# Optimization experiments

Measured on AMD Instinct MI355X. Metric: run time of the kernel, lower is better.

Reference implementation:

```python
import jax, jax.numpy as jnp
import numpy as np

N_TOKEN = 32000; N_LAYER = 6; N_HEAD = 16; D_MODEL = 1024; D_HEAD = 64; D_INNER = 4096
QLEN = 512; MEM_LEN = 512; BSZ = 4


def setup_inputs() -> dict:
    key = jax.random.key(0)
    ks = jax.random.split(key, 12)
    f = lambda k, shape: jax.random.normal(k, shape, dtype=jnp.float32) * 0.02
    return {
        'data': jax.random.randint(ks[0], (QLEN, BSZ), 0, N_TOKEN, dtype=jnp.int32),
        'target': jax.random.randint(ks[1], (QLEN, BSZ), 0, N_TOKEN, dtype=jnp.int32),
        'mems': jax.random.normal(ks[2], (N_LAYER + 1, MEM_LEN, BSZ, D_MODEL), dtype=jnp.float32),
        'emb_weight': f(ks[3], (N_TOKEN, D_MODEL)),        # tied input/output embedding
        'out_bias': jnp.zeros((N_TOKEN,), jnp.float32),
        'r_w_bias': f(ks[4], (N_HEAD, D_HEAD)),
        'r_r_bias': f(ks[5], (N_HEAD, D_HEAD)),
        'qkv_w': f(ks[6], (N_LAYER, 3 * N_HEAD * D_HEAD, D_MODEL)),  # bias=False in original
        'r_w': f(ks[7], (N_LAYER, N_HEAD * D_HEAD, D_MODEL)),        # r_net, bias=False
        'o_w': f(ks[8], (N_LAYER, D_MODEL, N_HEAD * D_HEAD)),        # o_net, bias=False
        'ln1_g': jnp.ones((N_LAYER, D_MODEL), jnp.float32),
        'ln1_b': jnp.zeros((N_LAYER, D_MODEL), jnp.float32),
        'ff1_w': f(ks[9], (N_LAYER, D_INNER, D_MODEL)),
        'ff1_b': jnp.zeros((N_LAYER, D_INNER), jnp.float32),
        'ff2_w': f(ks[10], (N_LAYER, D_MODEL, D_INNER)),
        'ff2_b': jnp.zeros((N_LAYER, D_MODEL), jnp.float32),
        'ln2_g': jnp.ones((N_LAYER, D_MODEL), jnp.float32),
        'ln2_b': jnp.zeros((N_LAYER, D_MODEL), jnp.float32),
    }


def _layernorm(x, g, b, eps=1e-5):
    mu = x.mean(-1, keepdims=True)
    var = ((x - mu) ** 2).mean(-1, keepdims=True)
    return (x - mu) * jax.lax.rsqrt(var + eps) * g + b


def _rel_shift(x):
    # x: (qlen, klen, bsz, n_head) -> TransformerXL relative shift
    q, k, b, h = x.shape
    x = jnp.concatenate([jnp.zeros((q, 1, b, h), x.dtype), x], axis=1)  # (q, k+1, b, h)
    return x.reshape(k + 1, q, b, h)[1:].reshape(q, k, b, h)


def _forward_core(data, target, mems, emb_weight, out_bias, r_w_bias, r_r_bias,
                  qkv_w, r_w, o_w, ln1_g, ln1_b, ff1_w, ff1_b, ff2_w, ff2_b, ln2_g, ln2_b):
    qlen, bsz = data.shape
    mlen = mems.shape[1]
    klen = mlen + qlen
    scale = 1.0 / (D_HEAD ** 0.5)

    # AdaptiveEmbedding with div_val=1, no cutoffs: plain lookup scaled by sqrt(d_model)
    h = emb_weight[data] * jnp.float32(D_MODEL ** 0.5)  # (qlen, bsz, d_model)

    # sinusoidal relative positions, descending klen-1 .. 0
    pos_seq = jnp.arange(klen - 1, -1, -1, dtype=jnp.float32)
    inv_freq = 1.0 / (10000.0 ** (jnp.arange(0, D_MODEL, 2, dtype=jnp.float32) / D_MODEL))
    sinusoid = pos_seq[:, None] * inv_freq[None, :]
    pos_emb = jnp.concatenate([jnp.sin(sinusoid), jnp.cos(sinusoid)], axis=-1)  # (klen, d_model)

    # causal mask shifted by memory length
    attn_mask = jnp.triu(jnp.ones((qlen, klen), bool), k=1 + mlen)
    NEG = jnp.float32(-1e30)

    for i in range(N_LAYER):
        cat = jnp.concatenate([mems[i], h], axis=0)              # (klen, b, d)
        heads = jnp.einsum('kbd,ed->kbe', cat, qkv_w[i])         # (klen, b, 3*H*dh)
        q, k_, v = jnp.split(heads, 3, axis=-1)
        q = q[-qlen:].reshape(qlen, bsz, N_HEAD, D_HEAD)
        k_ = k_.reshape(klen, bsz, N_HEAD, D_HEAD)
        v = v.reshape(klen, bsz, N_HEAD, D_HEAD)
        r = jnp.einsum('kd,ed->ke', pos_emb, r_w[i]).reshape(klen, N_HEAD, D_HEAD)

        AC = jnp.einsum('ibnd,jbnd->ijbn', q + r_w_bias, k_)     # content term
        BD = _rel_shift(jnp.einsum('ibnd,jnd->ijbn', q + r_r_bias, r))  # position term
        score = (AC + BD) * scale
        score = jnp.where(attn_mask[:, :, None, None], NEG, score)
        prob = jax.nn.softmax(score, axis=1)                     # over key axis j
        attn_vec = jnp.einsum('ijbn,jbnd->ibnd', prob, v).reshape(qlen, bsz, N_HEAD * D_HEAD)
        attn_out = jnp.einsum('ibe,de->ibd', attn_vec, o_w[i])
        h = _layernorm(h + attn_out, ln1_g[i], ln1_b[i])         # post-lnorm (pre_lnorm=False)

        ff_h = jax.nn.relu(jnp.einsum('ibd,fd->ibf', h, ff1_w[i]) + ff1_b[i])
        ff = jnp.einsum('ibf,df->ibd', ff_h, ff2_w[i]) + ff2_b[i]
        h = _layernorm(h + ff, ln2_g[i], ln2_b[i])

    # ProjectedAdaptiveLogSoftmax, no cutoffs, tied weight: plain softmax NLL
    logits = jnp.einsum('ibd,vd->ibv', h, emb_weight) + out_bias
    logp = jax.nn.log_softmax(logits, axis=-1)
    loss = -jnp.take_along_axis(logp, target[:, :, None].astype(jnp.int32), axis=-1)[:, :, 0]
    return loss  # (tgt_len, bsz)


def reference(data, target, mems, emb_weight, out_bias, r_w_bias, r_r_bias,
              qkv_w, r_w, o_w, ln1_g, ln1_b, ff1_w, ff1_b, ff2_w, ff2_b, ln2_g, ln2_b):
    return _forward_core(data, target, mems, emb_weight, out_bias, r_w_bias, r_r_bias,
                         qkv_w, r_w, o_w, ln1_g, ln1_b, ff1_w, ff1_b, ff2_w, ff2_b, ln2_g, ln2_b)
```

## Files before the change

kernel.cpp:

```cpp
#include <hip/hip_runtime.h>
#include <math.h>


typedef unsigned short u16;
typedef __attribute__((ext_vector_type(8))) short bf16x8;
typedef __attribute__((ext_vector_type(4))) float f32x4;

#define LINMOD (1 << 30)
constexpr int PITCH = 40;

__device__ __forceinline__ u16 f2bf(float f) {
    unsigned u = __float_as_uint(f);
    return (u16)((u + 0x7fffu + ((u >> 16) & 1u)) >> 16);
}
__device__ __forceinline__ float bf2f(u16 b) {
    return __uint_as_float((unsigned)b << 16);
}

template<int BM, int BN, int EPI>
__global__ __launch_bounds__(256)
void mgemm(const u16* __restrict__ A, int lda, long alo, long ahi, int amod,
           const u16* __restrict__ B, int ldb, long blo, long bhi, int bmod,
           void* __restrict__ Cv, int ldc, long clo, long chi, int cmod,
           const float* __restrict__ bias, int M, int N, int K, int relu)
{
    constexpr int WM = BM / 2, WN = BN / 2, MT = WM / 16, NT = WN / 16;
    __shared__ u16 As[BM * PITCH];
    __shared__ u16 Bs[BN * PITCH];
    const int z = blockIdx.z;
    A += (long)(z % amod) * alo + (long)(z / amod) * ahi;
    B += (long)(z % bmod) * blo + (long)(z / bmod) * bhi;
    const long coff = (long)(z % cmod) * clo + (long)(z / cmod) * chi;

    const int m0 = blockIdx.y * BM, n0 = blockIdx.x * BN;
    const int t = threadIdx.x;
    const int l = t & 63, w = t >> 6;
    const int wm = w >> 1, wn = w & 1;
    const int fr = l & 15, fq = l >> 4;

    f32x4 acc[MT][NT];
    #pragma unroll
    for (int i = 0; i < MT; ++i)
        #pragma unroll
        for (int j = 0; j < NT; ++j) acc[i][j] = (f32x4){0.f, 0.f, 0.f, 0.f};

    constexpr int AIT = BM * 4 / 256;
    constexpr int BIT = BN * 4 / 256;

    const int nk = K / 32;
    for (int kt = 0; kt < nk; ++kt) {
        uint4 av[AIT], bv[BIT];
        #pragma unroll
        for (int i = 0; i < AIT; ++i) {
            int c = t + i * 256, row = c >> 2, q = c & 3;
            av[i] = *(const uint4*)(A + (long)(m0 + row) * lda + kt * 32 + q * 8);
        }
        #pragma unroll
        for (int i = 0; i < BIT; ++i) {
            int c = t + i * 256, row = c >> 2, q = c & 3;
            bv[i] = *(const uint4*)(B + (long)(n0 + row) * ldb + kt * 32 + q * 8);
        }
        __syncthreads();
        #pragma unroll
        for (int i = 0; i < AIT; ++i) {
            int c = t + i * 256, row = c >> 2, q = c & 3;
            *(uint4*)&As[row * PITCH + q * 8] = av[i];
        }
        #pragma unroll
        for (int i = 0; i < BIT; ++i) {
            int c = t + i * 256, row = c >> 2, q = c & 3;
            *(uint4*)&Bs[row * PITCH + q * 8] = bv[i];
        }
        __syncthreads();
        bf16x8 af[MT], bfr[NT];
        #pragma unroll
        for (int i = 0; i < MT; ++i)
            af[i] = *(const bf16x8*)&As[(wm * WM + i * 16 + fr) * PITCH + fq * 8];
        #pragma unroll
        for (int j = 0; j < NT; ++j)
            bfr[j] = *(const bf16x8*)&Bs[(wn * WN + j * 16 + fr) * PITCH + fq * 8];
        #pragma unroll
        for (int i = 0; i < MT; ++i)
            #pragma unroll
            for (int j = 0; j < NT; ++j)
                acc[i][j] = __builtin_amdgcn_mfma_f32_16x16x32_bf16(
                    af[i], bfr[j], acc[i][j], 0, 0, 0);
    }

    if constexpr (EPI == 1) {
        u16* C = (u16*)Cv + coff;
        #pragma unroll
        for (int i = 0; i < MT; ++i) {
            int rb = m0 + wm * WM + i * 16 + fq * 4;
            #pragma unroll
            for (int j = 0; j < NT; ++j) {
                int gcol = n0 + wn * WN + j * 16 + fr;
                float bb = bias ? bias[gcol] : 0.f;
                #pragma unroll
                for (int r = 0; r < 4; ++r) {
                    float v = acc[i][j][r] + bb;
                    if (relu) v = fmaxf(v, 0.f);
                    C[(long)(rb + r) * ldc + gcol] = f2bf(v);
                }
            }
        }
    } else {
        float* C = (float*)Cv + coff;
        #pragma unroll
        for (int i = 0; i < MT; ++i) {
            int rb = m0 + wm * WM + i * 16 + fq * 4;
            #pragma unroll
            for (int j = 0; j < NT; ++j) {
                int gcol = n0 + wn * WN + j * 16 + fr;
                float bb = bias ? bias[gcol] : 0.f;
                #pragma unroll
                for (int r = 0; r < 4; ++r) {
                    float v = acc[i][j][r] + bb;
                    if (relu) v = fmaxf(v, 0.f);
                    C[(long)(rb + r) * ldc + gcol] = v;
                }
            }
        }
    }
}

template<int BM, int BN, int EPI>
static inline void mg(hipStream_t st,
    const u16* A, int lda, long alo, long ahi, int amod,
    const u16* B, int ldb, long blo, long bhi, int bmod,
    void* C, int ldc, long clo, long chi, int cmod,
    const float* bias, int M, int N, int K, int relu, int batch)
{
    dim3 grid(N / BN, M / BM, batch);
    mgemm<BM, BN, EPI><<<grid, 256, 0, st>>>(A, lda, alo, ahi, amod,
        B, ldb, blo, bhi, bmod, C, ldc, clo, chi, cmod, bias, M, N, K, relu);
}

__global__ __launch_bounds__(256)
void attn_kernel(const u16* __restrict__ qw, const u16* __restrict__ qr,
                 const u16* __restrict__ heads, const u16* __restrict__ rbuf,
                 u16* __restrict__ attnv)
{
    __shared__ u16 sm[80384];
    __shared__ float pmax[2][128];
    __shared__ float psum[2][128];
    u16* qw_s = sm;
    u16* qr_s = sm + 9216;
    u16* k_s  = sm + 18432;
    u16* r_s  = sm + 27648;
    u16* vT_s = sm + 36864;
    u16* bd0  = sm + 45568;
    u16* bd1  = sm + 62976;

    const int zz = blockIdx.x, b = zz >> 4, n = zz & 15;
    const int i0 = blockIdx.y * 128;
    const int t = threadIdx.x, l = t & 63, w = t >> 6;
    const int fr = l & 15, fq = l >> 4, wm = w >> 1, wn = w & 1;

    const u16* qwg = qw + (long)zz * 32768 + (long)i0 * 64;
    const u16* qrg = qr + (long)zz * 32768 + (long)i0 * 64;
    {
        int jr0 = 384 - i0;
        #pragma unroll
        for (int it = 0; it < 4; ++it) {
            int idx = t + it * 256, row = idx >> 3, q8 = idx & 7;
            *(uint4*)&qw_s[row * 72 + q8 * 8] = *(const uint4*)&qwg[row * 64 + q8 * 8];
            *(uint4*)&qr_s[row * 72 + q8 * 8] = *(const uint4*)&qrg[row * 64 + q8 * 8];
            *(uint4*)&r_s[row * 72 + q8 * 8] =
                *(const uint4*)&rbuf[(long)(jr0 + row) * 1024 + n * 64 + q8 * 8];
        }
    }
    __syncthreads();

    auto computeBD = [&](u16* out) {
        f32x4 bacc[4][4];
        #pragma unroll
        for (int i = 0; i < 4; ++i)
            #pragma unroll
            for (int j = 0; j < 4; ++j) bacc[i][j] = (f32x4){0.f, 0.f, 0.f, 0.f};
        #pragma unroll
        for (int ks = 0; ks < 2; ++ks) {
            bf16x8 af[4], bfr[4];
            #pragma unroll
            for (int i = 0; i < 4; ++i)
                af[i] = *(const bf16x8*)&qr_s[(wm * 64 + i * 16 + fr) * 72 + ks * 32 + fq * 8];
            #pragma unroll
            for (int j = 0; j < 4; ++j)
                bfr[j] = *(const bf16x8*)&r_s[(wn * 64 + j * 16 + fr) * 72 + ks * 32 + fq * 8];
            #pragma unroll
            for (int i = 0; i < 4; ++i)
                #pragma unroll
                for (int j = 0; j < 4; ++j)
                    bacc[i][j] = __builtin_amdgcn_mfma_f32_16x16x32_bf16(
                        af[i], bfr[j], bacc[i][j], 0, 0, 0);
        }
        #pragma unroll
        for (int i = 0; i < 4; ++i)
            #pragma unroll
            for (int j = 0; j < 4; ++j)
                #pragma unroll
                for (int r = 0; r < 4; ++r)
                    out[(wm * 64 + i * 16 + fq * 4 + r) * 136 + wn * 64 + j * 16 + fr] =
                        f2bf(bacc[i][j][r]);
    };
    computeBD(bd0);

    float m_st[4][4], l_st[4][4];
    #pragma unroll
    for (int i = 0; i < 4; ++i)
        #pragma unroll
        for (int r = 0; r < 4; ++r) { m_st[i][r] = -3e38f; l_st[i][r] = 0.f; }
    f32x4 Oa[4][2];
    #pragma unroll
    for (int i = 0; i < 4; ++i)
        #pragma unroll
        for (int j = 0; j < 2; ++j) Oa[i][j] = (f32x4){0.f, 0.f, 0.f, 0.f};

    const int ntiles = (640 + i0) >> 7;
    for (int tt = 0; tt < ntiles; ++tt) {
        const int j0 = tt << 7;
        const int jr0b = j0 - i0 + 512;
        u16* bda = (tt & 1) ? bd1 : bd0;
        u16* bdb = (tt & 1) ? bd0 : bd1;

        __syncthreads();

        #pragma unroll
        for (int it = 0; it < 4; ++it) {
            int idx = t + it * 256, row = idx >> 3, q8 = idx & 7;
            long hb = ((long)(j0 + row) * 4 + b) * 3072 + n * 64 + q8 * 8;
            *(uint4*)&k_s[row * 72 + q8 * 8] = *(const uint4*)&heads[hb + 1024];
            uint4 vv = *(const uint4*)&heads[hb + 2048];
            u16 vt[8]; *(uint4*)vt = vv;
            #pragma unroll
            for (int d = 0; d < 8; ++d) vT_s[(q8 * 8 + d) * 136 + row] = vt[d];
            if (jr0b < 1024)
                *(uint4*)&r_s[row * 72 + q8 * 8] =
                    *(const uint4*)&rbuf[(long)(jr0b + row) * 1024 + n * 64 + q8 * 8];
        }
        __syncthreads();

        if (jr0b < 1024) computeBD(bdb);

        f32x4 acc[4][4];
        #pragma unroll
        for (int i = 0; i < 4; ++i)
            #pragma unroll
            for (int j = 0; j < 4; ++j) acc[i][j] = (f32x4){0.f, 0.f, 0.f, 0.f};
        #pragma unroll
        for (int ks = 0; ks < 2; ++ks) {
            bf16x8 af[4], bfr[4];
            #pragma unroll
            for (int i = 0; i < 4; ++i)
                af[i] = *(const bf16x8*)&qw_s[(wm * 64 + i * 16 + fr) * 72 + ks * 32 + fq * 8];
            #pragma unroll
            for (int j = 0; j < 4; ++j)
                bfr[j] = *(const bf16x8*)&k_s[(wn * 64 + j * 16 + fr) * 72 + ks * 32 + fq * 8];
            #pragma unroll
            for (int i = 0; i < 4; ++i)
                #pragma unroll
                for (int j = 0; j < 4; ++j)
                    acc[i][j] = __builtin_amdgcn_mfma_f32_16x16x32_bf16(
                        af[i], bfr[j], acc[i][j], 0, 0, 0);
        }
        __syncthreads();

        const int Dl = j0 - i0;
        float rm[4][4];
        #pragma unroll
        for (int i = 0; i < 4; ++i)
            #pragma unroll
            for (int r = 0; r < 4; ++r) rm[i][r] = -3e38f;
        #pragma unroll
        for (int i = 0; i < 4; ++i) {
            #pragma unroll
            for (int r = 0; r < 4; ++r) {
                int ii = wm * 64 + i * 16 + fq * 4 + r;
                #pragma unroll
                for (int j = 0; j < 4; ++j) {
                    int jj = wn * 64 + j * 16 + fr;
                    int d = jj - ii;
                    int idx = 127 + d;
                    u16 bv = (idx < 128) ? bda[ii * 136 + idx] : bdb[ii * 136 + idx - 128];
                    float sv = (acc[i][j][r] + bf2f(bv)) * 0.125f;
                    sv = (Dl + d > 512) ? -1e30f : sv;
                    acc[i][j][r] = sv;
                    rm[i][r] = fmaxf(rm[i][r], sv);
                }
            }
        }
        #pragma unroll
        for (int i = 0; i < 4; ++i)
            #pragma unroll
            for (int r = 0; r < 4; ++r) {
                float v = rm[i][r];
                v = fmaxf(v, __shfl_xor(v, 1, 64));
                v = fmaxf(v, __shfl_xor(v, 2, 64));
                v = fmaxf(v, __shfl_xor(v, 4, 64));
                v = fmaxf(v, __shfl_xor(v, 8, 64));
                rm[i][r] = v;
            }
        if (fr == 0) {
            #pragma unroll
            for (int i = 0; i < 4; ++i)
                #pragma unroll
                for (int r = 0; r < 4; ++r)
                    pmax[wn][wm * 64 + i * 16 + fq * 4 + r] = rm[i][r];
        }
        __syncthreads();

        float alpha[4][4];
        #pragma unroll
        for (int i = 0; i < 4; ++i)
            #pragma unroll
            for (int r = 0; r < 4; ++r) {
                int row = wm * 64 + i * 16 + fq * 4 + r;
                float tm = fmaxf(pmax[0][row], pmax[1][row]);
                float mn = fmaxf(m_st[i][r], tm);
                alpha[i][r] = __expf(m_st[i][r] - mn);
                m_st[i][r] = mn;
            }
        u16* Pp = bda;
        float rs[4][4];
        #pragma unroll
        for (int i = 0; i < 4; ++i)
            #pragma unroll
            for (int r = 0; r < 4; ++r) rs[i][r] = 0.f;
        #pragma unroll
        for (int i = 0; i < 4; ++i) {
            #pragma unroll
            for (int r = 0; r < 4; ++r) {
                int row = wm * 64 + i * 16 + fq * 4 + r;
                #pragma unroll
                for (int j = 0; j < 4; ++j) {
                    float p = __expf(acc[i][j][r] - m_st[i][r]);
                    rs[i][r] += p;
                    Pp[row * 136 + wn * 64 + j * 16 + fr] = f2bf(p);
                }
            }
        }
        #pragma unroll
        for (int i = 0; i < 4; ++i)
            #pragma unroll
            for (int r = 0; r < 4; ++r) {
                float v = rs[i][r];
                v += __shfl_xor(v, 1, 64);
                v += __shfl_xor(v, 2, 64);
                v += __shfl_xor(v, 4, 64);
                v += __shfl_xor(v, 8, 64);
                rs[i][r] = v;
            }
        if (fr == 0) {
            #pragma unroll
            for (int i = 0; i < 4; ++i)
                #pragma unroll
                for (int r = 0; r < 4; ++r)
                    psum[wn][wm * 64 + i * 16 + fq * 4 + r] = rs[i][r];
        }
        #pragma unroll
        for (int i = 0; i < 4; ++i)
            #pragma unroll
            for (int j = 0; j < 2; ++j)
                #pragma unroll
                for (int r = 0; r < 4; ++r) Oa[i][j][r] *= alpha[i][r];
        __syncthreads();

        #pragma unroll
        for (int i = 0; i < 4; ++i)
            #pragma unroll
            for (int r = 0; r < 4; ++r) {
                int row = wm * 64 + i * 16 + fq * 4 + r;
                l_st[i][r] = alpha[i][r] * l_st[i][r] + psum[0][row] + psum[1][row];
            }
        #pragma unroll
        for (int ks = 0; ks < 4; ++ks) {
            bf16x8 pa[4], vb[2];
            #pragma unroll
            for (int i = 0; i < 4; ++i)
                pa[i] = *(const bf16x8*)&Pp[(wm * 64 + i * 16 + fr) * 136 + ks * 32 + fq * 8];
            #pragma unroll
            for (int j = 0; j < 2; ++j)
                vb[j] = *(const bf16x8*)&vT_s[(wn * 32 + j * 16 + fr) * 136 + ks * 32 + fq * 8];
            #pragma unroll
            for (int i = 0; i < 4; ++i)
                #pragma unroll
                for (int j = 0; j < 2; ++j)
                    Oa[i][j] = __builtin_amdgcn_mfma_f32_16x16x32_bf16(
                        pa[i], vb[j], Oa[i][j], 0, 0, 0);
        }
    }

    #pragma unroll
    for (int i = 0; i < 4; ++i) {
        #pragma unroll
        for (int r = 0; r < 4; ++r) {
            int gi = i0 + wm * 64 + i * 16 + fq * 4 + r;
            float inv = 1.0f / l_st[i][r];
            #pragma unroll
            for (int j = 0; j < 2; ++j) {
                int col = n * 64 + wn * 32 + j * 16 + fr;
                attnv[((long)gi * 4 + b) * 1024 + col] = f2bf(Oa[i][j][r] * inv);
            }
        }
    }
}


__device__ __forceinline__ float blk_sum(float v, float* smv) {
    #pragma unroll
    for (int m = 32; m; m >>= 1) v += __shfl_xor(v, m, 64);
    int lane = threadIdx.x & 63, w = threadIdx.x >> 6;
    if (lane == 0) smv[w] = v;
    __syncthreads();
    v = smv[0] + smv[1] + smv[2] + smv[3];
    __syncthreads();
    return v;
}

__device__ __forceinline__ float blk_max(float v, float* smv) {
    #pragma unroll
    for (int m = 32; m; m >>= 1) v = fmaxf(v, __shfl_xor(v, m, 64));
    int lane = threadIdx.x & 63, w = threadIdx.x >> 6;
    if (lane == 0) smv[w] = v;
    __syncthreads();
    v = fmaxf(fmaxf(smv[0], smv[1]), fmaxf(smv[2], smv[3]));
    __syncthreads();
    return v;
}

__global__ __launch_bounds__(256)
void f2b_kernel(const float* __restrict__ in, u16* __restrict__ out, int n4)
{
    int i = blockIdx.x * 256 + threadIdx.x;
    if (i >= n4) return;
    float4 v = ((const float4*)in)[i];
    uint2 o;
    o.x = (unsigned)f2bf(v.x) | ((unsigned)f2bf(v.y) << 16);
    o.y = (unsigned)f2bf(v.z) | ((unsigned)f2bf(v.w) << 16);
    ((uint2*)out)[i] = o;
}

__global__ __launch_bounds__(256)
void cat_kernel(const float* __restrict__ memsl, const float* __restrict__ h,
                u16* __restrict__ cat)
{
    int i = blockIdx.x * 256 + threadIdx.x;
    float4 v = (i < 524288) ? ((const float4*)memsl)[i]
                            : ((const float4*)h)[i - 524288];
    uint2 o;
    o.x = (unsigned)f2bf(v.x) | ((unsigned)f2bf(v.y) << 16);
    o.y = (unsigned)f2bf(v.z) | ((unsigned)f2bf(v.w) << 16);
    ((uint2*)cat)[i] = o;
}

__global__ __launch_bounds__(256)
void embed_kernel(const int* __restrict__ data, const float* __restrict__ emb,
                  float* __restrict__ h)
{
    long idx = (long)blockIdx.x * 256 + threadIdx.x;
    int r = (int)(idx >> 10), d = (int)(idx & 1023);
    h[idx] = emb[(long)data[r] * 1024 + d] * 32.0f;
}

__global__ __launch_bounds__(256)
void posemb_kernel(u16* __restrict__ pe)
{
    int idx = blockIdx.x * 256 + threadIdx.x;
    int p = idx >> 10, d = idx & 1023;
    float pos = (float)(1023 - p);
    int j = d & 511;
    float invf = powf(10000.0f, -(float)j * (1.0f / 512.0f));
    float a = pos * invf;
    pe[idx] = f2bf((d < 512) ? sinf(a) : cosf(a));
}

__global__ __launch_bounds__(256)
void qwqr_kernel(const u16* __restrict__ heads, const float* __restrict__ rwb,
                 const float* __restrict__ rrb, u16* __restrict__ qw,
                 u16* __restrict__ qr)
{
    int idx = blockIdx.x * 256 + threadIdx.x;
    int d = idx & 63, i = (idx >> 6) & 511, n = (idx >> 15) & 15, b = idx >> 19;
    float v = bf2f(heads[(long)((512 + i) * 4 + b) * 3072 + n * 64 + d]);
    int e = n * 64 + d;
    qw[idx] = f2bf(v + rwb[e]);
    qr[idx] = f2bf(v + rrb[e]);
}

__global__ __launch_bounds__(256)
void add_ln_kernel(float* __restrict__ h, const float* __restrict__ res,
                   const float* __restrict__ g, const float* __restrict__ be)
{
    __shared__ float smv[4];
    int row = blockIdx.x, t = threadIdx.x;
    float* hp = h + (long)row * 1024;
    float4 x = *(float4*)(hp + t * 4);
    float4 rv = *(const float4*)(res + (long)row * 1024 + t * 4);
    x.x += rv.x; x.y += rv.y; x.z += rv.z; x.w += rv.w;
    float s = blk_sum(x.x + x.y + x.z + x.w, smv);
    float mu = s * (1.0f / 1024.0f);
    float d0 = x.x - mu, d1 = x.y - mu, d2 = x.z - mu, d3 = x.w - mu;
    float s2 = blk_sum(d0 * d0 + d1 * d1 + d2 * d2 + d3 * d3, smv);
    float inv = rsqrtf(s2 * (1.0f / 1024.0f) + 1e-5f);
    float4 gg = *(const float4*)(g + t * 4);
    float4 bb = *(const float4*)(be + t * 4);
    float4 o;
    o.x = d0 * inv * gg.x + bb.x;
    o.y = d1 * inv * gg.y + bb.y;
    o.z = d2 * inv * gg.z + bb.z;
    o.w = d3 * inv * gg.w + bb.w;
    *(float4*)(hp + t * 4) = o;
}

__global__ void init_ms_kernel(float2* __restrict__ ms)
{
    int i = blockIdx.x * 256 + threadIdx.x;
    if (i < 2048) ms[i] = make_float2(-3e38f, 0.f);
}

__global__ __launch_bounds__(256)
void merge_kernel(const float* __restrict__ chunk, float2* __restrict__ ms, int CN)
{
    __shared__ float smv[4];
    int row = blockIdx.x, t = threadIdx.x;
    const float* cp = chunk + (long)row * CN;
    float m = -3e38f;
    for (int j = t; j < CN; j += 256) m = fmaxf(m, cp[j]);
    m = blk_max(m, smv);
    float s = 0.f;
    for (int j = t; j < CN; j += 256) s += __expf(cp[j] - m);
    s = blk_sum(s, smv);
    if (t == 0) {
        float2 cur = ms[row];
        float nm = fmaxf(cur.x, m);
        ms[row] = make_float2(nm, cur.y * __expf(cur.x - nm) + s * __expf(m - nm));
    }
}

__global__ __launch_bounds__(256)
void final_kernel(const float* __restrict__ h, const float* __restrict__ emb,
                  const float* __restrict__ ob, const int* __restrict__ target,
                  const float2* __restrict__ ms, float* __restrict__ out)
{
    __shared__ float smv[4];
    int row = blockIdx.x, t = threadIdx.x;
    int tok = target[row];
    const float* hp = h + (long)row * 1024;
    const float* ep = emb + (long)tok * 1024;
    float4 a = *(const float4*)(hp + t * 4);
    float4 b = *(const float4*)(ep + t * 4);
    float s = blk_sum(a.x * b.x + a.y * b.y + a.z * b.z + a.w * b.w, smv);
    if (t == 0) {
        float2 v = ms[row];
        out[row] = v.x + logf(v.y) - (s + ob[tok]);
    }
}


extern "C" void kernel_launch(void* const* d_in, const int* in_sizes, int n_in,
                              void* d_out, int out_size, void* d_ws, size_t ws_size,
                              hipStream_t stream)
{
    const int*   data     = (const int*)d_in[0];
    const int*   target   = (const int*)d_in[1];
    const float* mems     = (const float*)d_in[2];
    const float* emb      = (const float*)d_in[3];
    const float* out_bias = (const float*)d_in[4];
    const float* r_w_bias = (const float*)d_in[5];
    const float* r_r_bias = (const float*)d_in[6];
    const float* qkv_w    = (const float*)d_in[7];
    const float* r_w      = (const float*)d_in[8];
    const float* o_w      = (const float*)d_in[9];
    const float* ln1_g    = (const float*)d_in[10];
    const float* ln1_b    = (const float*)d_in[11];
    const float* ff1_w    = (const float*)d_in[12];
    const float* ff1_b    = (const float*)d_in[13];
    const float* ff2_w    = (const float*)d_in[14];
    const float* ff2_b    = (const float*)d_in[15];
    const float* ln2_g    = (const float*)d_in[16];
    const float* ln2_b    = (const float*)d_in[17];
    float* out = (float*)d_out;
    float* ws  = (float*)d_ws;

    float* h       = ws;
    float* tmp     = ws + 2097152;
    u16*  pe_bf    = (u16*)(ws + 4194304);
    u16*  rbuf_bf  = (u16*)(ws + 4718592);
    u16*  cat_bf   = (u16*)(ws + 5242880);
    u16*  heads_bf = (u16*)(ws + 7340032);
    u16*  qw_bf    = (u16*)(ws + 13631488);
    u16*  qr_bf    = (u16*)(ws + 14680064);
    u16*  attnv_bf = (u16*)(ws + 15728640);
    u16*  h_bf     = (u16*)(ws + 16777216);
    u16*  wqkv     = (u16*)(ws + 17825792);
    u16*  wr       = wqkv + 3145728;
    u16*  wo       = wr + 1048576;
    u16*  wf1      = wo + 1048576;
    u16*  wf2      = wf1 + 4194304;
    float* big     = ws + 24641536;
    float2* ms     = (float2*)(ws + 58195968);
    u16*  ffh_bf   = (u16*)big;
    float* chunk   = big;
    u16*  embc_bf  = (u16*)(big + 16777216);

    embed_kernel<<<8192, 256, 0, stream>>>(data, emb, h);
    posemb_kernel<<<4096, 256, 0, stream>>>(pe_bf);

    for (int l = 0; l < 6; ++l) {
        f2b_kernel<<<3072, 256, 0, stream>>>(qkv_w + (size_t)l * 3145728, wqkv, 786432);
        f2b_kernel<<<1024, 256, 0, stream>>>(r_w + (size_t)l * 1048576, wr, 262144);
        f2b_kernel<<<1024, 256, 0, stream>>>(o_w + (size_t)l * 1048576, wo, 262144);
        f2b_kernel<<<4096, 256, 0, stream>>>(ff1_w + (size_t)l * 4194304, wf1, 1048576);
        f2b_kernel<<<4096, 256, 0, stream>>>(ff2_w + (size_t)l * 4194304, wf2, 1048576);
        cat_kernel<<<4096, 256, 0, stream>>>(mems + (size_t)l * 2097152, h, cat_bf);

        mg<128,128,1>(stream, cat_bf, 1024, 0, 0, LINMOD, wqkv, 1024, 0, 0, LINMOD,
                      heads_bf, 3072, 0, 0, LINMOD, nullptr, 4096, 3072, 1024, 0, 1);
        mg<64,64,1>(stream, pe_bf, 1024, 0, 0, LINMOD, wr, 1024, 0, 0, LINMOD,
                    rbuf_bf, 1024, 0, 0, LINMOD, nullptr, 1024, 1024, 1024, 0, 1);

        qwqr_kernel<<<8192, 256, 0, stream>>>(heads_bf, r_w_bias, r_r_bias, qw_bf, qr_bf);

        attn_kernel<<<dim3(64, 4), 256, 0, stream>>>(qw_bf, qr_bf, heads_bf,
                                                     rbuf_bf, attnv_bf);

        mg<64,64,0>(stream, attnv_bf, 1024, 0, 0, LINMOD, wo, 1024, 0, 0, LINMOD,
                    tmp, 1024, 0, 0, LINMOD, nullptr, 2048, 1024, 1024, 0, 1);

        add_ln_kernel<<<2048, 256, 0, stream>>>(h, tmp, ln1_g + l * 1024, ln1_b + l * 1024);
        f2b_kernel<<<2048, 256, 0, stream>>>(h, h_bf, 524288);

        mg<64,64,1>(stream, h_bf, 1024, 0, 0, LINMOD, wf1, 1024, 0, 0, LINMOD,
                    ffh_bf, 4096, 0, 0, LINMOD, ff1_b + l * 4096, 2048, 4096, 1024, 1, 1);
        mg<64,64,0>(stream, ffh_bf, 4096, 0, 0, LINMOD, wf2, 4096, 0, 0, LINMOD,
                    tmp, 1024, 0, 0, LINMOD, ff2_b + l * 1024, 2048, 1024, 4096, 0, 1);

        add_ln_kernel<<<2048, 256, 0, stream>>>(h, tmp, ln2_g + l * 1024, ln2_b + l * 1024);
    }

    f2b_kernel<<<2048, 256, 0, stream>>>(h, h_bf, 524288);
    init_ms_kernel<<<8, 256, 0, stream>>>(ms);

    const int chunkN[4] = {8192, 8192, 8192, 7424};
    long off = 0;
    for (int c = 0; c < 4; ++c) {
        int CN = chunkN[c];
        int n4 = CN * 1024 / 4;
        f2b_kernel<<<(n4 + 255) / 256, 256, 0, stream>>>(emb + off * 1024, embc_bf, n4);
        mg<128,128,0>(stream, h_bf, 1024, 0, 0, LINMOD, embc_bf, 1024, 0, 0, LINMOD,
                      chunk, CN, 0, 0, LINMOD, out_bias + off, 2048, CN, 1024, 0, 1);
        merge_kernel<<<2048, 256, 0, stream>>>(chunk, ms, CN);
        off += CN;
    }
    final_kernel<<<2048, 256, 0, stream>>>(h, emb, out_bias, target, ms, out);
}
```

Measured before the change: 3.482 ms.

## Fuse logits softmax partials into GEMM epilogue, retile GEMMs, add XCD swizzle

Adds a GEMM epilogue that reduces each 128-column logit tile to a per-row (max, sum-exp) pair. The full fp32 logits matrix is no longer written and reread in four chunks, and a small lse_kernel merges the 250 partials per row. It also enlarges tiles for the o/ff1/ff2 GEMMs and adds an XCD-aware workgroup remap for better L2 locality across MI355X chiplets. The whole embedding is now converted to bf16 in one pass, which needs a larger workspace region.

```diff
diff --git a/kernel.cpp b/kernel.cpp
--- a/kernel.cpp
+++ b/kernel.cpp
@@ -22,7 +22,7 @@
 void mgemm(const u16* __restrict__ A, int lda, long alo, long ahi, int amod,
            const u16* __restrict__ B, int ldb, long blo, long bhi, int bmod,
            void* __restrict__ Cv, int ldc, long clo, long chi, int cmod,
-           const float* __restrict__ bias, int M, int N, int K, int relu)
+           const float* __restrict__ bias, int M, int N, int K, int relu, int swz)
 {
     constexpr int WM = BM / 2, WN = BN / 2, MT = WM / 16, NT = WN / 16;
     __shared__ u16 As[BM * PITCH];
@@ -32,7 +32,16 @@
     B += (long)(z % bmod) * blo + (long)(z / bmod) * bhi;
     const long coff = (long)(z % cmod) * clo + (long)(z / cmod) * chi;
 
-    const int m0 = blockIdx.y * BM, n0 = blockIdx.x * BN;
+    int bx = blockIdx.x, by = blockIdx.y;
+    if (swz) {
+        int nwg = gridDim.x * gridDim.y;
+        int flat = by * gridDim.x + bx;
+        int q = nwg >> 3, rr = nwg & 7, xcd = flat & 7, idx = flat >> 3;
+        int wgid = (xcd < rr ? xcd * (q + 1) : rr * (q + 1) + (xcd - rr) * q) + idx;
+        by = wgid % gridDim.y;
+        bx = wgid / gridDim.y;
+    }
+    const int m0 = by * BM, n0 = bx * BN;
     const int t = threadIdx.x;
     const int l = t & 63, w = t >> 6;
     const int wm = w >> 1, wn = w & 1;
@@ -104,7 +113,7 @@
                 }
             }
         }
-    } else {
+    } else if constexpr (EPI == 0) {
         float* C = (float*)Cv + coff;
         #pragma unroll
         for (int i = 0; i < MT; ++i) {
@@ -121,6 +130,46 @@
                 }
             }
         }
+    } else {
+        __shared__ float pm[2][BM];
+        __shared__ float ps[2][BM];
+        float bb[NT];
+        #pragma unroll
+        for (int j = 0; j < NT; ++j)
+            bb[j] = bias ? bias[n0 + wn * WN + j * 16 + fr] : 0.f;
+        #pragma unroll
+        for (int i = 0; i < MT; ++i) {
+            #pragma unroll
+            for (int r = 0; r < 4; ++r) {
+                float mx = -3e38f;
+                #pragma unroll
+                for (int j = 0; j < NT; ++j) mx = fmaxf(mx, acc[i][j][r] + bb[j]);
+                mx = fmaxf(mx, __shfl_xor(mx, 1, 64));
+                mx = fmaxf(mx, __shfl_xor(mx, 2, 64));
+                mx = fmaxf(mx, __shfl_xor(mx, 4, 64));
+                mx = fmaxf(mx, __shfl_xor(mx, 8, 64));
+                float s = 0.f;
+                #pragma unroll
+                for (int j = 0; j < NT; ++j) s += __expf(acc[i][j][r] + bb[j] - mx);
+                s += __shfl_xor(s, 1, 64);
+                s += __shfl_xor(s, 2, 64);
+                s += __shfl_xor(s, 4, 64);
+                s += __shfl_xor(s, 8, 64);
+                if (fr == 0) {
+                    int row = wm * WM + i * 16 + fq * 4 + r;
+                    pm[wn][row] = mx;
+                    ps[wn][row] = s;
+                }
+            }
+        }
+        __syncthreads();
+        if (t < BM && (m0 + t) < M) {
+            float ma = pm[0][t], mb = pm[1][t];
+            float m = fmaxf(ma, mb);
+            float s = ps[0][t] * __expf(ma - m) + ps[1][t] * __expf(mb - m);
+            float2* P = (float2*)Cv;
+            P[(long)(m0 + t) * gridDim.x + bx] = make_float2(m, s);
+        }
     }
 }
 
@@ -129,11 +178,11 @@
     const u16* A, int lda, long alo, long ahi, int amod,
     const u16* B, int ldb, long blo, long bhi, int bmod,
     void* C, int ldc, long clo, long chi, int cmod,
-    const float* bias, int M, int N, int K, int relu, int batch)
+    const float* bias, int M, int N, int K, int relu, int batch, int swz)
 {
     dim3 grid(N / BN, M / BM, batch);
     mgemm<BM, BN, EPI><<<grid, 256, 0, st>>>(A, lda, alo, ahi, amod,
-        B, ldb, blo, bhi, bmod, C, ldc, clo, chi, cmod, bias, M, N, K, relu);
+        B, ldb, blo, bhi, bmod, C, ldc, clo, chi, cmod, bias, M, N, K, relu, swz);
 }
 
 __global__ __launch_bounds__(256)
@@ -512,29 +561,22 @@
     *(float4*)(hp + t * 4) = o;
 }
 
-__global__ void init_ms_kernel(float2* __restrict__ ms)
-{
-    int i = blockIdx.x * 256 + threadIdx.x;
-    if (i < 2048) ms[i] = make_float2(-3e38f, 0.f);
-}
-
-__global__ __launch_bounds__(256)
-void merge_kernel(const float* __restrict__ chunk, float2* __restrict__ ms, int CN)
+__global__ __launch_bounds__(256)
+void lse_kernel(const float2* __restrict__ part, int nblk, float2* __restrict__ ms)
 {
     __shared__ float smv[4];
     int row = blockIdx.x, t = threadIdx.x;
-    const float* cp = chunk + (long)row * CN;
+    const float2* pp = part + (long)row * nblk;
     float m = -3e38f;
-    for (int j = t; j < CN; j += 256) m = fmaxf(m, cp[j]);
+    for (int j = t; j < nblk; j += 256) m = fmaxf(m, pp[j].x);
     m = blk_max(m, smv);
     float s = 0.f;
-    for (int j = t; j < CN; j += 256) s += __expf(cp[j] - m);
+    for (int j = t; j < nblk; j += 256) {
+        float2 p = pp[j];
+        s += p.y * __expf(p.x - m);
+    }
     s = blk_sum(s, smv);
-    if (t == 0) {
-        float2 cur = ms[row];
-        float nm = fmaxf(cur.x, m);
-        ms[row] = make_float2(nm, cur.y * __expf(cur.x - nm) + s * __expf(m - nm));
-    }
+    if (t == 0) ms[row] = make_float2(m, s);
 }
 
 __global__ __launch_bounds__(256)
@@ -600,8 +642,8 @@
     float* big     = ws + 24641536;
     float2* ms     = (float2*)(ws + 58195968);
     u16*  ffh_bf   = (u16*)big;
-    float* chunk   = big;
-    u16*  embc_bf  = (u16*)(big + 16777216);
+    u16*  embc_bf  = (u16*)big;
+    float2* partials = (float2*)(big + 16777216);
 
     embed_kernel<<<8192, 256, 0, stream>>>(data, emb, h);
     posemb_kernel<<<4096, 256, 0, stream>>>(pe_bf);
@@ -615,42 +657,35 @@
         cat_kernel<<<4096, 256, 0, stream>>>(mems + (size_t)l * 2097152, h, cat_bf);
 
         mg<128,128,1>(stream, cat_bf, 1024, 0, 0, LINMOD, wqkv, 1024, 0, 0, LINMOD,
-                      heads_bf, 3072, 0, 0, LINMOD, nullptr, 4096, 3072, 1024, 0, 1);
+                      heads_bf, 3072, 0, 0, LINMOD, nullptr, 4096, 3072, 1024, 0, 1, 1);
         mg<64,64,1>(stream, pe_bf, 1024, 0, 0, LINMOD, wr, 1024, 0, 0, LINMOD,
-                    rbuf_bf, 1024, 0, 0, LINMOD, nullptr, 1024, 1024, 1024, 0, 1);
+                    rbuf_bf, 1024, 0, 0, LINMOD, nullptr, 1024, 1024, 1024, 0, 1, 0);
 
         qwqr_kernel<<<8192, 256, 0, stream>>>(heads_bf, r_w_bias, r_r_bias, qw_bf, qr_bf);
 
         attn_kernel<<<dim3(64, 4), 256, 0, stream>>>(qw_bf, qr_bf, heads_bf,
                                                      rbuf_bf, attnv_bf);
 
-        mg<64,64,0>(stream, attnv_bf, 1024, 0, 0, LINMOD, wo, 1024, 0, 0, LINMOD,
-                    tmp, 1024, 0, 0, LINMOD, nullptr, 2048, 1024, 1024, 0, 1);
+        mg<128,64,0>(stream, attnv_bf, 1024, 0, 0, LINMOD, wo, 1024, 0, 0, LINMOD,
+                     tmp, 1024, 0, 0, LINMOD, nullptr, 2048, 1024, 1024, 0, 1, 1);
 
         add_ln_kernel<<<2048, 256, 0, stream>>>(h, tmp, ln1_g + l * 1024, ln1_b + l * 1024);
         f2b_kernel<<<2048, 256, 0, stream>>>(h, h_bf, 524288);
 
-        mg<64,64,1>(stream, h_bf, 1024, 0, 0, LINMOD, wf1, 1024, 0, 0, LINMOD,
-                    ffh_bf, 4096, 0, 0, LINMOD, ff1_b + l * 4096, 2048, 4096, 1024, 1, 1);
-        mg<64,64,0>(stream, ffh_bf, 4096, 0, 0, LINMOD, wf2, 4096, 0, 0, LINMOD,
-                    tmp, 1024, 0, 0, LINMOD, ff2_b + l * 1024, 2048, 1024, 4096, 0, 1);
+        mg<128,128,1>(stream, h_bf, 1024, 0, 0, LINMOD, wf1, 1024, 0, 0, LINMOD,
+                      ffh_bf, 4096, 0, 0, LINMOD, ff1_b + l * 4096, 2048, 4096, 1024, 1, 1, 1);
+        mg<128,64,0>(stream, ffh_bf, 4096, 0, 0, LINMOD, wf2, 4096, 0, 0, LINMOD,
+                     tmp, 1024, 0, 0, LINMOD, ff2_b + l * 1024, 2048, 1024, 4096, 0, 1, 1);
 
         add_ln_kernel<<<2048, 256, 0, stream>>>(h, tmp, ln2_g + l * 1024, ln2_b + l * 1024);
     }
 
     f2b_kernel<<<2048, 256, 0, stream>>>(h, h_bf, 524288);
-    init_ms_kernel<<<8, 256, 0, stream>>>(ms);
-
-    const int chunkN[4] = {8192, 8192, 8192, 7424};
-    long off = 0;
-    for (int c = 0; c < 4; ++c) {
-        int CN = chunkN[c];
-        int n4 = CN * 1024 / 4;
-        f2b_kernel<<<(n4 + 255) / 256, 256, 0, stream>>>(emb + off * 1024, embc_bf, n4);
-        mg<128,128,0>(stream, h_bf, 1024, 0, 0, LINMOD, embc_bf, 1024, 0, 0, LINMOD,
-                      chunk, CN, 0, 0, LINMOD, out_bias + off, 2048, CN, 1024, 0, 1);
-        merge_kernel<<<2048, 256, 0, stream>>>(chunk, ms, CN);
-        off += CN;
-    }
+    f2b_kernel<<<32000, 256, 0, stream>>>(emb, embc_bf, 8192000);
+
+    mg<128,128,2>(stream, h_bf, 1024, 0, 0, LINMOD, embc_bf, 1024, 0, 0, LINMOD,
+                  partials, 0, 0, 0, LINMOD, out_bias, 2048, 32000, 1024, 0, 1, 1);
+
+    lse_kernel<<<2048, 256, 0, stream>>>(partials, 250, ms);
     final_kernel<<<2048, 256, 0, stream>>>(h, emb, out_bias, target, ms, out);
 }
```

Measured after the change: 4.140 ms. 1.19x slower.
